# Optimization experiments

Measured on AMD Instinct MI355X. Metric: run time of the kernel, lower is better.

Reference implementation:

```python
import jax, jax.numpy as jnp
import numpy as np

NEG_INF = -9e15  # matches torch's -9000000000000000.0 mask value
LEAKY_SLOPE = 0.2  # init alpha


def setup_inputs() -> dict:
    key = jax.random.key(0)
    k1, k2, k3, k4 = jax.random.split(key, 4)
    N, dim = 4096, 128
    hidden = jax.random.normal(k1, (N, dim), dtype=jnp.float32)
    adj = jax.random.randint(k2, (N, N), 0, 5)  # relation codes 0..4
    W = jax.random.normal(k3, (4, dim), dtype=jnp.float32) * (1.0 / np.sqrt(dim))
    b = jax.random.normal(k4, (4,), dtype=jnp.float32) * 0.01
    return {"hidden": hidden, "adj": adj, "W": W, "b": b}


def reference(hidden, adj, W, b):
    # e_k[i,j] = leakyrelu(sum_d h[i,d]*h[j,d]*W[k,d] + b[k])
    # equivalent to the torch repeat/view outer-product + four dim->1 Linears,
    # computed without materializing the [N,N,dim] intermediate.
    hw = hidden[None, :, :] * W[:, None, :]               # [4, N, dim]
    e = jnp.einsum('knd,md->knm', hw, hidden) + b[:, None, None]  # [4, N, N]
    e = jax.nn.leaky_relu(e, negative_slope=LEAKY_SLOPE)
    neg = jnp.asarray(NEG_INF, dtype=e.dtype)
    alpha = jnp.where(adj == 1, e[0], neg)
    alpha = jnp.where(adj == 2, e[1], alpha)
    alpha = jnp.where(adj == 3, e[2], alpha)
    alpha = jnp.where(adj == 4, e[3], alpha)
    alpha = jax.nn.softmax(alpha, axis=-1)                # [N, N]
    return alpha @ hidden                                  # [N, dim]
```

## Files before the change

### kernel.cpp

```cpp
#include <hip/hip_runtime.h>

#define NN 4096
#define DIM 128
#define TN 32
#define TM 128
#define NTILES 16

typedef __attribute__((ext_vector_type(8))) short bf16x8;
typedef __attribute__((ext_vector_type(4))) float f32x4;

#define LSTRIDE 136
#define REGION  (128 * LSTRIDE)
#define TILE_USH (2 * REGION)
#define TILE_CHUNKS 68
#define PST 136

__device__ inline unsigned short f2bf(float x) {
    union { float f; unsigned u; } v; v.f = x;
    unsigned r = v.u + 0x7FFFu + ((v.u >> 16) & 1u);
    return (unsigned short)(r >> 16);
}

__device__ inline void dma16(const void* g, void* l) {
    __builtin_amdgcn_global_load_lds(
        (const __attribute__((address_space(1))) void*)g,
        (__attribute__((address_space(3))) void*)l,
        16, 0, 0);
}

__global__ __launch_bounds__(256) void prep_pack_kernel(
    const float* __restrict__ hidden,
    unsigned short* __restrict__ Hpack)
{
    __shared__ unsigned short T[128 * LSTRIDE];
    const int tid = threadIdx.x;
    const int t0  = blockIdx.x;
    const int m0  = t0 * TM;
    unsigned short* rowdst = Hpack + (size_t)t0 * TILE_USH;
    unsigned short* coldst = rowdst + REGION;

    #pragma unroll
    for (int it = 0; it < 16; ++it) {
        int idx = tid + 256 * it;
        int row = idx >> 5;
        int c4  = (idx & 31) * 4;
        float4 v = *(const float4*)(hidden + (size_t)(m0 + row) * DIM + c4);
        ushort4 o;
        o.x = f2bf(v.x); o.y = f2bf(v.y); o.z = f2bf(v.z); o.w = f2bf(v.w);
        *(ushort4*)(rowdst + row * LSTRIDE + c4) = o;
        T[(c4 + 0) * LSTRIDE + row] = o.x;
        T[(c4 + 1) * LSTRIDE + row] = o.y;
        T[(c4 + 2) * LSTRIDE + row] = o.z;
        T[(c4 + 3) * LSTRIDE + row] = o.w;
    }
    __syncthreads();
    #pragma unroll
    for (int it = 0; it < 8; ++it) {
        int idx = tid + 256 * it;
        int d  = idx >> 4;
        int c8 = (idx & 15) * 8;
        uint4 v = *(const uint4*)(T + d * LSTRIDE + c8);
        *(uint4*)(coldst + d * LSTRIDE + c8) = v;
    }
}

__global__ __launch_bounds__(256) void prep_adj_kernel(
    const int* __restrict__ adj, unsigned char* __restrict__ adjp)
{
    const int p   = blockIdx.x;
    const int nb  = p >> 5, gt = p & 31;
    const int tid = threadIdx.x;
    const int m   = tid >> 1;
    const int rh  = (tid & 1) * 16;
    unsigned char bytes[16];
    #pragma unroll
    for (int rr = 0; rr < 16; ++rr)
        bytes[rr] = (unsigned char)adj[(size_t)(nb * 32 + rh + rr) * NN + gt * 128 + m];
    *(uint4*)(adjp + (size_t)p * 4096 + m * 32 + rh) = *(const uint4*)bytes;
}

__global__ __launch_bounds__(512, 2) void gat_flash_kernel(
    const float* __restrict__ hidden,
    const unsigned short* __restrict__ Hpack,
    const unsigned char* __restrict__ adjp,
    const float* __restrict__ W,
    const float* __restrict__ bvec,
    float*       __restrict__ Opart,
    float*       __restrict__ lpart)
{
    __shared__ __align__(16) unsigned short HH[2][TILE_USH];
    __shared__ __align__(16) unsigned short Plc[TN * PST];
    __shared__ float redsum[8][16];

    const int tid  = threadIdx.x;
    const int w    = tid >> 6;
    const int lane = tid & 63;
    const int g    = lane >> 4;
    const int l15  = lane & 15;
    const int blk  = blockIdx.x;
    const int nb   = blk >> 1;
    const int half = blk & 1;
    const int n0   = nb * TN;
    const int gt0  = half * NTILES;
    const int rg   = w >> 2;
    const int ms   = w & 3;
    const int lofs = lane * 16;
    const float NEG = -9.0e15f;

    const float b0 = bvec[0], b1 = bvec[1], b2 = bvec[2], b3 = bvec[3];

    {
        const char* src = (const char*)(Hpack + (size_t)gt0 * TILE_USH);
        char* dst = (char*)&HH[0][0];
        #pragma unroll
        for (int it = 0; it < 9; ++it) {
            int chunk = it * 8 + w;
            if (chunk < TILE_CHUNKS)
                dma16(src + chunk * 1024 + lofs, dst + chunk * 1024);
        }
    }
    {
        int qr = tid >> 2;
        int r  = qr & 31;
        int d0 = (tid & 3) * 32;
        const float* hrow = hidden + (size_t)(n0 + r) * DIM + d0;
        const float* wrow = W + (qr >> 5) * DIM + d0;
        unsigned short* qdst = &HH[1][qr * LSTRIDE + d0];
        #pragma unroll
        for (int c = 0; c < 8; ++c) {
            float4 hv = *(const float4*)(hrow + 4 * c);
            float4 wv = *(const float4*)(wrow + 4 * c);
            ushort4 o;
            o.x = f2bf(hv.x * wv.x); o.y = f2bf(hv.y * wv.y);
            o.z = f2bf(hv.z * wv.z); o.w = f2bf(hv.w * wv.w);
            *(ushort4*)(qdst + 4 * c) = o;
        }
    }
    __syncthreads();

    bf16x8 Af[4][4];
    #pragma unroll
    for (int k = 0; k < 4; ++k)
        #pragma unroll
        for (int ks = 0; ks < 4; ++ks)
            Af[k][ks] = *(const bf16x8*)&HH[1][(k * 32 + rg * 16 + l15) * LSTRIDE + ks * 32 + 8 * g];
    __syncthreads();

    float lrow[4] = {0.f, 0.f, 0.f, 0.f};
    f32x4 Oacc[2];
    Oacc[0] = (f32x4){0.f, 0.f, 0.f, 0.f};
    Oacc[1] = (f32x4){0.f, 0.f, 0.f, 0.f};

    const unsigned char* apb = adjp + (size_t)(nb * 32 + gt0) * 4096;
    uchar4 av4[2], avn4[2];
    av4[0] = *(const uchar4*)&apb[(ms * 32 + l15) * 32 + rg * 16 + 4 * g];
    av4[1] = *(const uchar4*)&apb[(ms * 32 + 16 + l15) * 32 + rg * 16 + 4 * g];

    for (int tile = 0; tile < NTILES; ++tile) {
        const int cur = tile & 1;
        const int nxt = cur ^ 1;

        if (tile + 1 < NTILES) {
            const char* src = (const char*)(Hpack + (size_t)(gt0 + tile + 1) * TILE_USH);
            char* dst = (char*)&HH[nxt][0];
            #pragma unroll
            for (int it = 0; it < 9; ++it) {
                int chunk = it * 8 + w;
                if (chunk < TILE_CHUNKS)
                    dma16(src + chunk * 1024 + lofs, dst + chunk * 1024);
            }
            const unsigned char* apn = apb + (size_t)(tile + 1) * 4096;
            avn4[0] = *(const uchar4*)&apn[(ms * 32 + l15) * 32 + rg * 16 + 4 * g];
            avn4[1] = *(const uchar4*)&apn[(ms * 32 + 16 + l15) * 32 + rg * 16 + 4 * g];
        }

        f32x4 S[4][2];
        #pragma unroll
        for (int k = 0; k < 4; ++k) {
            S[k][0] = (f32x4){0.f, 0.f, 0.f, 0.f};
            S[k][1] = (f32x4){0.f, 0.f, 0.f, 0.f};
        }
        #pragma unroll
        for (int ks = 0; ks < 4; ++ks) {
            #pragma unroll
            for (int ch = 0; ch < 2; ++ch) {
                bf16x8 B = *(const bf16x8*)&HH[cur][(ms * 32 + ch * 16 + l15) * LSTRIDE + ks * 32 + 8 * g];
                #pragma unroll
                for (int k = 0; k < 4; ++k)
                    S[k][ch] = __builtin_amdgcn_mfma_f32_16x16x32_bf16(Af[k][ks], B, S[k][ch], 0, 0, 0);
            }
        }

        #pragma unroll
        for (int ch = 0; ch < 2; ++ch) {
            const unsigned char* ab = (const unsigned char*)&av4[ch];
            #pragma unroll
            for (int t = 0; t < 4; ++t) {
                int a = ab[t];
                float s = S[0][ch][t] + b0;
                s = (a == 2) ? S[1][ch][t] + b1 : s;
                s = (a == 3) ? S[2][ch][t] + b2 : s;
                s = (a == 4) ? S[3][ch][t] + b3 : s;
                float e = fmaxf(s, 0.2f * s);
                e = (a == 0) ? NEG : e;
                float p = __expf(e);
                lrow[t] += p;
                Plc[(rg * 16 + 4 * g + t) * PST + ms * 32 + ch * 16 + l15] = f2bf(p);
            }
        }

        asm volatile("s_waitcnt lgkmcnt(0)\n\ts_barrier" ::: "memory");

        #pragma unroll
        for (int c4 = 0; c4 < 4; ++c4) {
            bf16x8 Pa = *(const bf16x8*)&Plc[(rg * 16 + l15) * PST + c4 * 32 + 8 * g];
            #pragma unroll
            for (int dt = 0; dt < 2; ++dt) {
                bf16x8 Bv = *(const bf16x8*)&HH[cur][REGION + (ms * 32 + dt * 16 + l15) * LSTRIDE + c4 * 32 + 8 * g];
                Oacc[dt] = __builtin_amdgcn_mfma_f32_16x16x32_bf16(Pa, Bv, Oacc[dt], 0, 0, 0);
            }
        }

        av4[0] = avn4[0]; av4[1] = avn4[1];
        __syncthreads();
    }

    #pragma unroll
    for (int t = 0; t < 4; ++t) {
        float v = lrow[t];
        v += __shfl_xor(v, 1); v += __shfl_xor(v, 2);
        v += __shfl_xor(v, 4); v += __shfl_xor(v, 8);
        if (l15 == 0) redsum[w][4 * g + t] = v;
    }
    __syncthreads();
    if (tid < 32) {
        int rgp = tid >> 4, rr = tid & 15;
        float s = redsum[rgp * 4 + 0][rr] + redsum[rgp * 4 + 1][rr]
                + redsum[rgp * 4 + 2][rr] + redsum[rgp * 4 + 3][rr];
        lpart[blk * 32 + tid] = s;
    }
    float* Ob = Opart + (size_t)blk * TN * DIM;
    #pragma unroll
    for (int dt = 0; dt < 2; ++dt)
        #pragma unroll
        for (int t = 0; t < 4; ++t)
            Ob[(rg * 16 + 4 * g + t) * DIM + ms * 32 + dt * 16 + l15] = Oacc[dt][t];
}

__global__ __launch_bounds__(256) void combine_kernel(
    const float* __restrict__ Opart, const float* __restrict__ lpart,
    float* __restrict__ out)
{
    int idx = blockIdx.x * 256 + threadIdx.x;
    int r = idx >> 7, d = idx & 127;
    int nb = r >> 5, rr = r & 31;
    float O0 = Opart[(size_t)(nb * 2) * (TN * DIM) + rr * 128 + d];
    float O1 = Opart[(size_t)(nb * 2 + 1) * (TN * DIM) + rr * 128 + d];
    float l0 = lpart[(nb * 2) * 32 + rr];
    float l1 = lpart[(nb * 2 + 1) * 32 + rr];
    out[idx] = (O0 + O1) / (l0 + l1);
}

extern "C" void kernel_launch(void* const* d_in, const int* in_sizes, int n_in,
                              void* d_out, int out_size, void* d_ws, size_t ws_size,
                              hipStream_t stream) {
    const float* hidden = (const float*)d_in[0];
    const int*   adj    = (const int*)d_in[1];
    const float* W      = (const float*)d_in[2];
    const float* b      = (const float*)d_in[3];
    float* out = (float*)d_out;

    char* ws = (char*)d_ws;
    unsigned short* Hpack = (unsigned short*)ws;
    unsigned char*  adjp  = (unsigned char*)(ws + (4u << 20));
    float* Opart = (float*)(ws + (20u << 20));
    float* lpart = (float*)(ws + (24u << 20));

    prep_pack_kernel<<<NN / TM, 256, 0, stream>>>(hidden, Hpack);
    prep_adj_kernel<<<128 * 32, 256, 0, stream>>>(adj, adjp);
    gat_flash_kernel<<<256, 512, 0, stream>>>(hidden, Hpack, adjp, W, b, Opart, lpart);
    combine_kernel<<<NN * DIM / 256, 256, 0, stream>>>(Opart, lpart, out);
}
```

Baseline: 152.5 us.

## Drop adjacency prepack, read int adj directly, split columns four ways with smaller tiles

Removes the separate adjacency repacking kernel and has the flash kernel read the int32 adjacency directly, with each lane loading 16 contiguous columns per row. Column tiles shrink from 128 to 64 and the column range is split across four blocks instead of two. This doubles the grid to 512 blocks and raises the occupancy hint to 4 blocks per CU. The goal is to avoid a full extra pass over the 64MB adjacency and to get more parallelism. The trade-offs are a 4-way partial combine, more per-tile barrier overhead relative to MFMA work, and wider adjacency loads inside the main loop.

```diff
diff --git a/kernel.cpp b/kernel.cpp
--- a/kernel.cpp
+++ b/kernel.cpp
@@ -3,17 +3,20 @@
 #define NN 4096
 #define DIM 128
 #define TN 32
-#define TM 128
+#define TM 64
 #define NTILES 16
+#define NSPLIT 4
 
 typedef __attribute__((ext_vector_type(8))) short bf16x8;
 typedef __attribute__((ext_vector_type(4))) float f32x4;
 
 #define LSTRIDE 136
-#define REGION  (128 * LSTRIDE)
-#define TILE_USH (2 * REGION)
-#define TILE_CHUNKS 68
-#define PST 136
+#define HCST    72
+#define HROW_USH (TM * LSTRIDE)
+#define HCOL_USH (DIM * HCST)
+#define TILE_USH (HROW_USH + HCOL_USH)
+#define TILE_CHUNKS 35
+#define PST 72
 
 __device__ inline unsigned short f2bf(float x) {
     union { float f; unsigned u; } v; v.f = x;
@@ -32,15 +35,15 @@
     const float* __restrict__ hidden,
     unsigned short* __restrict__ Hpack)
 {
-    __shared__ unsigned short T[128 * LSTRIDE];
+    __shared__ unsigned short T[DIM * HCST];
     const int tid = threadIdx.x;
     const int t0  = blockIdx.x;
     const int m0  = t0 * TM;
     unsigned short* rowdst = Hpack + (size_t)t0 * TILE_USH;
-    unsigned short* coldst = rowdst + REGION;
-
-    #pragma unroll
-    for (int it = 0; it < 16; ++it) {
+    unsigned short* coldst = rowdst + HROW_USH;
+
+    #pragma unroll
+    for (int it = 0; it < 8; ++it) {
         int idx = tid + 256 * it;
         int row = idx >> 5;
         int c4  = (idx & 31) * 4;
@@ -48,41 +51,26 @@
         ushort4 o;
         o.x = f2bf(v.x); o.y = f2bf(v.y); o.z = f2bf(v.z); o.w = f2bf(v.w);
         *(ushort4*)(rowdst + row * LSTRIDE + c4) = o;
-        T[(c4 + 0) * LSTRIDE + row] = o.x;
-        T[(c4 + 1) * LSTRIDE + row] = o.y;
-        T[(c4 + 2) * LSTRIDE + row] = o.z;
-        T[(c4 + 3) * LSTRIDE + row] = o.w;
-    }
-    __syncthreads();
-    #pragma unroll
-    for (int it = 0; it < 8; ++it) {
+        T[(c4 + 0) * HCST + row] = o.x;
+        T[(c4 + 1) * HCST + row] = o.y;
+        T[(c4 + 2) * HCST + row] = o.z;
+        T[(c4 + 3) * HCST + row] = o.w;
+    }
+    __syncthreads();
+    #pragma unroll
+    for (int it = 0; it < 4; ++it) {
         int idx = tid + 256 * it;
-        int d  = idx >> 4;
-        int c8 = (idx & 15) * 8;
-        uint4 v = *(const uint4*)(T + d * LSTRIDE + c8);
-        *(uint4*)(coldst + d * LSTRIDE + c8) = v;
-    }
-}
-
-__global__ __launch_bounds__(256) void prep_adj_kernel(
-    const int* __restrict__ adj, unsigned char* __restrict__ adjp)
-{
-    const int p   = blockIdx.x;
-    const int nb  = p >> 5, gt = p & 31;
-    const int tid = threadIdx.x;
-    const int m   = tid >> 1;
-    const int rh  = (tid & 1) * 16;
-    unsigned char bytes[16];
-    #pragma unroll
-    for (int rr = 0; rr < 16; ++rr)
-        bytes[rr] = (unsigned char)adj[(size_t)(nb * 32 + rh + rr) * NN + gt * 128 + m];
-    *(uint4*)(adjp + (size_t)p * 4096 + m * 32 + rh) = *(const uint4*)bytes;
-}
-
-__global__ __launch_bounds__(512, 2) void gat_flash_kernel(
+        int d  = idx >> 3;
+        int c8 = (idx & 7) * 8;
+        uint4 v = *(const uint4*)(T + d * HCST + c8);
+        *(uint4*)(coldst + d * HCST + c8) = v;
+    }
+}
+
+__global__ __launch_bounds__(512, 4) void gat_flash_kernel(
     const float* __restrict__ hidden,
     const unsigned short* __restrict__ Hpack,
-    const unsigned char* __restrict__ adjp,
+    const int*   __restrict__ adj,
     const float* __restrict__ W,
     const float* __restrict__ bvec,
     float*       __restrict__ Opart,
@@ -98,10 +86,10 @@
     const int g    = lane >> 4;
     const int l15  = lane & 15;
     const int blk  = blockIdx.x;
-    const int nb   = blk >> 1;
-    const int half = blk & 1;
+    const int nb   = blk >> 2;
+    const int qtr  = blk & 3;
     const int n0   = nb * TN;
-    const int gt0  = half * NTILES;
+    const int gt0  = qtr * NTILES;
     const int rg   = w >> 2;
     const int ms   = w & 3;
     const int lofs = lane * 16;
@@ -113,7 +101,7 @@
         const char* src = (const char*)(Hpack + (size_t)gt0 * TILE_USH);
         char* dst = (char*)&HH[0][0];
         #pragma unroll
-        for (int it = 0; it < 9; ++it) {
+        for (int it = 0; it < 5; ++it) {
             int chunk = it * 8 + w;
             if (chunk < TILE_CHUNKS)
                 dma16(src + chunk * 1024 + lofs, dst + chunk * 1024);
@@ -151,10 +139,10 @@
     Oacc[0] = (f32x4){0.f, 0.f, 0.f, 0.f};
     Oacc[1] = (f32x4){0.f, 0.f, 0.f, 0.f};
 
-    const unsigned char* apb = adjp + (size_t)(nb * 32 + gt0) * 4096;
-    uchar4 av4[2], avn4[2];
-    av4[0] = *(const uchar4*)&apb[(ms * 32 + l15) * 32 + rg * 16 + 4 * g];
-    av4[1] = *(const uchar4*)&apb[(ms * 32 + 16 + l15) * 32 + rg * 16 + 4 * g];
+    int avc[4], avn[4];
+    #pragma unroll
+    for (int t = 0; t < 4; ++t)
+        avc[t] = adj[(size_t)(n0 + rg * 16 + 4 * g + t) * NN + gt0 * TM + ms * 16 + l15];
 
     for (int tile = 0; tile < NTILES; ++tile) {
         const int cur = tile & 1;
@@ -164,64 +152,55 @@
             const char* src = (const char*)(Hpack + (size_t)(gt0 + tile + 1) * TILE_USH);
             char* dst = (char*)&HH[nxt][0];
             #pragma unroll
-            for (int it = 0; it < 9; ++it) {
+            for (int it = 0; it < 5; ++it) {
                 int chunk = it * 8 + w;
                 if (chunk < TILE_CHUNKS)
                     dma16(src + chunk * 1024 + lofs, dst + chunk * 1024);
             }
-            const unsigned char* apn = apb + (size_t)(tile + 1) * 4096;
-            avn4[0] = *(const uchar4*)&apn[(ms * 32 + l15) * 32 + rg * 16 + 4 * g];
-            avn4[1] = *(const uchar4*)&apn[(ms * 32 + 16 + l15) * 32 + rg * 16 + 4 * g];
-        }
-
-        f32x4 S[4][2];
-        #pragma unroll
-        for (int k = 0; k < 4; ++k) {
-            S[k][0] = (f32x4){0.f, 0.f, 0.f, 0.f};
-            S[k][1] = (f32x4){0.f, 0.f, 0.f, 0.f};
-        }
+            #pragma unroll
+            for (int t = 0; t < 4; ++t)
+                avn[t] = adj[(size_t)(n0 + rg * 16 + 4 * g + t) * NN + (gt0 + tile + 1) * TM + ms * 16 + l15];
+        }
+
+        f32x4 S[4];
+        #pragma unroll
+        for (int k = 0; k < 4; ++k) S[k] = (f32x4){0.f, 0.f, 0.f, 0.f};
         #pragma unroll
         for (int ks = 0; ks < 4; ++ks) {
-            #pragma unroll
-            for (int ch = 0; ch < 2; ++ch) {
-                bf16x8 B = *(const bf16x8*)&HH[cur][(ms * 32 + ch * 16 + l15) * LSTRIDE + ks * 32 + 8 * g];
-                #pragma unroll
-                for (int k = 0; k < 4; ++k)
-                    S[k][ch] = __builtin_amdgcn_mfma_f32_16x16x32_bf16(Af[k][ks], B, S[k][ch], 0, 0, 0);
-            }
-        }
-
-        #pragma unroll
-        for (int ch = 0; ch < 2; ++ch) {
-            const unsigned char* ab = (const unsigned char*)&av4[ch];
-            #pragma unroll
-            for (int t = 0; t < 4; ++t) {
-                int a = ab[t];
-                float s = S[0][ch][t] + b0;
-                s = (a == 2) ? S[1][ch][t] + b1 : s;
-                s = (a == 3) ? S[2][ch][t] + b2 : s;
-                s = (a == 4) ? S[3][ch][t] + b3 : s;
-                float e = fmaxf(s, 0.2f * s);
-                e = (a == 0) ? NEG : e;
-                float p = __expf(e);
-                lrow[t] += p;
-                Plc[(rg * 16 + 4 * g + t) * PST + ms * 32 + ch * 16 + l15] = f2bf(p);
-            }
+            bf16x8 B = *(const bf16x8*)&HH[cur][(ms * 16 + l15) * LSTRIDE + ks * 32 + 8 * g];
+            #pragma unroll
+            for (int k = 0; k < 4; ++k)
+                S[k] = __builtin_amdgcn_mfma_f32_16x16x32_bf16(Af[k][ks], B, S[k], 0, 0, 0);
+        }
+
+        #pragma unroll
+        for (int t = 0; t < 4; ++t) {
+            int a = avc[t];
+            float s = S[0][t] + b0;
+            s = (a == 2) ? S[1][t] + b1 : s;
+            s = (a == 3) ? S[2][t] + b2 : s;
+            s = (a == 4) ? S[3][t] + b3 : s;
+            float e = fmaxf(s, 0.2f * s);
+            e = (a == 0) ? NEG : e;
+            float p = __expf(e);
+            lrow[t] += p;
+            Plc[(rg * 16 + 4 * g + t) * PST + ms * 16 + l15] = f2bf(p);
         }
 
         asm volatile("s_waitcnt lgkmcnt(0)\n\ts_barrier" ::: "memory");
 
         #pragma unroll
-        for (int c4 = 0; c4 < 4; ++c4) {
+        for (int c4 = 0; c4 < 2; ++c4) {
             bf16x8 Pa = *(const bf16x8*)&Plc[(rg * 16 + l15) * PST + c4 * 32 + 8 * g];
             #pragma unroll
             for (int dt = 0; dt < 2; ++dt) {
-                bf16x8 Bv = *(const bf16x8*)&HH[cur][REGION + (ms * 32 + dt * 16 + l15) * LSTRIDE + c4 * 32 + 8 * g];
+                bf16x8 Bv = *(const bf16x8*)&HH[cur][HROW_USH + (ms * 32 + dt * 16 + l15) * HCST + c4 * 32 + 8 * g];
                 Oacc[dt] = __builtin_amdgcn_mfma_f32_16x16x32_bf16(Pa, Bv, Oacc[dt], 0, 0, 0);
             }
         }
 
-        av4[0] = avn4[0]; av4[1] = avn4[1];
+        #pragma unroll
+        for (int t = 0; t < 4; ++t) avc[t] = avn[t];
         __syncthreads();
     }
 
@@ -254,11 +233,13 @@
     int idx = blockIdx.x * 256 + threadIdx.x;
     int r = idx >> 7, d = idx & 127;
     int nb = r >> 5, rr = r & 31;
-    float O0 = Opart[(size_t)(nb * 2) * (TN * DIM) + rr * 128 + d];
-    float O1 = Opart[(size_t)(nb * 2 + 1) * (TN * DIM) + rr * 128 + d];
-    float l0 = lpart[(nb * 2) * 32 + rr];
-    float l1 = lpart[(nb * 2 + 1) * 32 + rr];
-    out[idx] = (O0 + O1) / (l0 + l1);
+    float O = 0.f, l = 0.f;
+    #pragma unroll
+    for (int q = 0; q < NSPLIT; ++q) {
+        O += Opart[(size_t)(nb * NSPLIT + q) * (TN * DIM) + rr * 128 + d];
+        l += lpart[(nb * NSPLIT + q) * 32 + rr];
+    }
+    out[idx] = O / l;
 }
 
 extern "C" void kernel_launch(void* const* d_in, const int* in_sizes, int n_in,
@@ -272,12 +253,10 @@
 
     char* ws = (char*)d_ws;
     unsigned short* Hpack = (unsigned short*)ws;
-    unsigned char*  adjp  = (unsigned char*)(ws + (4u << 20));
-    float* Opart = (float*)(ws + (20u << 20));
-    float* lpart = (float*)(ws + (24u << 20));
+    float* Opart = (float*)(ws + (4u << 20));
+    float* lpart = (float*)(ws + (12u << 20));
 
     prep_pack_kernel<<<NN / TM, 256, 0, stream>>>(hidden, Hpack);
-    prep_adj_kernel<<<128 * 32, 256, 0, stream>>>(adj, adjp);
-    gat_flash_kernel<<<256, 512, 0, stream>>>(hidden, Hpack, adjp, W, b, Opart, lpart);
+    gat_flash_kernel<<<512, 512, 0, stream>>>(hidden, Hpack, adj, W, b, Opart, lpart);
     combine_kernel<<<NN * DIM / 256, 256, 0, stream>>>(Opart, lpart, out);
 }
```

New measurement: 149.5 us. 1.02x faster.
